# Optimization experiments

Measured on AMD Instinct MI355X. Metric: run time of the kernel, lower is better.

## Reference

```python
import jax, jax.numpy as jnp
import numpy as np

B = 1048576  # batch
A = 3        # number of actors in the ensemble


def _linear_params(key, out_d, in_d):
    """Stacked-over-actors torch.nn.Linear-style init: U(-1/sqrt(in), 1/sqrt(in))."""
    k1, k2 = jax.random.split(key)
    s = 1.0 / np.sqrt(in_d)
    W = jax.random.uniform(k1, (A, out_d, in_d), minval=-s, maxval=s, dtype=jnp.float32)
    b = jax.random.uniform(k2, (A, out_d), minval=-s, maxval=s, dtype=jnp.float32)
    return W, b


def setup_inputs() -> dict:
    key = jax.random.key(0)
    ks = jax.random.split(key, 10)
    spatial = jax.random.normal(ks[0], (B, 3, 9), dtype=jnp.float32)
    car_stats = jax.random.normal(ks[1], (B, 4), dtype=jnp.float32)  # unused by the model
    Wmx, bmx = _linear_params(ks[2], 10, 6)
    Wnx, bnx = _linear_params(ks[3], 10, 3)
    Wmy, bmy = _linear_params(ks[4], 10, 6)
    Wny, bny = _linear_params(ks[5], 10, 3)
    Wmz, bmz = _linear_params(ks[6], 5, 6)
    Wnz, bnz = _linear_params(ks[7], 5, 3)
    Wlin, blin = _linear_params(ks[8], 25, 25)
    Wout, bout = _linear_params(ks[9], 15, 25)
    return {
        "spatial": spatial, "car_stats": car_stats,
        "Wmx": Wmx, "bmx": bmx, "Wnx": Wnx, "bnx": bnx,
        "Wmy": Wmy, "bmy": bmy, "Wny": Wny, "bny": bny,
        "Wmz": Wmz, "bmz": bmz, "Wnz": Wnz, "bnz": bnz,
        "Wlin": Wlin, "blin": blin, "Wout": Wout, "bout": bout,
    }


def reference(spatial, car_stats,
              Wmx, bmx, Wnx, bnx,
              Wmy, bmy, Wny, bny,
              Wmz, bmz, Wnz, bnz,
              Wlin, blin, Wout, bout):
    # SimpleSpatialInput vectorized over the actor axis 'a':
    # (Linear(6->size)(s[:, :6])) * (Linear(3->size)(s[:, 6:9]))
    def proc(s, Wm, bm, Wn, bn):
        m = jnp.einsum('bi,aoi->bao', s[:, :6], Wm) + bm   # [B, A, size]
        n = jnp.einsum('bi,aoi->bao', s[:, 6:9], Wn) + bn  # [B, A, size]
        return m * n

    px = proc(spatial[:, 0], Wmx, bmx, Wnx, bnx)  # [B, A, 10]
    py = proc(spatial[:, 1], Wmy, bmy, Wny, bny)  # [B, A, 10]
    pz = proc(spatial[:, 2], Wmz, bmz, Wnz, bnz)  # [B, A, 5]
    ps = jnp.concatenate([px, py, pz], axis=-1)   # [B, A, 25]

    h = jnp.einsum('bad,aod->bao', ps, Wlin) + blin  # [B, A, 25]
    h = h / (1.0 + jnp.abs(h))                       # Softsign
    out = jnp.einsum('bad,aod->bao', h, Wout) + bout # [B, A, 15]

    result = jnp.transpose(out, (0, 2, 1))           # [B, 15, A] (stack dim=2)
    multiplier = jax.nn.softmax(result[:, 9, :], axis=1)  # [B, A]
    # stack of result[:, i] * multiplier over i=0..8, cumsum over actors,
    # take last -> plain weighted sum over the actor axis.
    return jnp.einsum('boa,ba->bo', result[:, :9, :], multiplier)  # [B, 9]
```

## Files before the change

### kernel.cpp

```cpp
#include <hip/hip_runtime.h>


typedef _Float16 half8  __attribute__((ext_vector_type(8)));
typedef float    floatx4 __attribute__((ext_vector_type(4)));

#define NFRAG 21
#define FRAG_HALFS (NFRAG * 512)
#define BIAS_FLOATS (NFRAG * 16)

__global__ __launch_bounds__(256) void prep_frags(
    const float* __restrict__ Wmx, const float* __restrict__ bmx,
    const float* __restrict__ Wnx, const float* __restrict__ bnx,
    const float* __restrict__ Wmy, const float* __restrict__ bmy,
    const float* __restrict__ Wny, const float* __restrict__ bny,
    const float* __restrict__ Wmz, const float* __restrict__ bmz,
    const float* __restrict__ Wnz, const float* __restrict__ bnz,
    const float* __restrict__ Wlin, const float* __restrict__ blin,
    const float* __restrict__ Wout, const float* __restrict__ bout,
    _Float16* __restrict__ frag, float* __restrict__ bias)
{
    int i = threadIdx.x + blockIdx.x * blockDim.x;
    if (i < FRAG_HALFS) {
        int f = i >> 9, rem = i & 511;
        int lane = rem >> 3, j = rem & 7;
        int q = lane >> 4, m = lane & 15;
        int a = f / 7, idx = f % 7;
        float v = 0.f;
        if (idx < 4) {
            int c = m + ((idx & 1) ? 16 : 0);
            int k = 8 * q + j;
            bool npart = (idx >= 2);
            if (c < 10) {
                if (!npart) { if (k < 6)             v = Wmx[(a*10 + c)*6 + k]; }
                else        { if (k >= 6 && k < 9)   v = Wnx[(a*10 + c)*3 + (k-6)]; }
            } else if (c < 20) {
                if (!npart) { if (k >= 9 && k < 15)  v = Wmy[(a*10 + c-10)*6 + (k-9)]; }
                else        { if (k >= 15 && k < 18) v = Wny[(a*10 + c-10)*3 + (k-15)]; }
            } else if (c < 25) {
                if (!npart) { if (k >= 18 && k < 24) v = Wmz[(a*5 + c-20)*6 + (k-18)]; }
                else        { if (k >= 24 && k < 27) v = Wnz[(a*5 + c-20)*3 + (k-24)]; }
            }
        } else if (idx < 6) {
            int o  = m + ((idx == 5) ? 16 : 0);
            int kc = 16 * (j >> 2) + 4 * q + (j & 3);
            if (o < 25 && kc < 25) v = Wlin[(a*25 + o)*25 + kc];
        } else {
            int ko = 16 * (j >> 2) + 4 * q + (j & 3);
            if (m < 10 && ko < 25) v = Wout[(a*15 + m)*25 + ko];
        }
        frag[(size_t)f * 512 + lane * 8 + j] = (_Float16)v;
    } else if (i < FRAG_HALFS + BIAS_FLOATS) {
        int r = i - FRAG_HALFS;
        int f = r >> 4, m = r & 15;
        int a = f / 7, idx = f % 7;
        float b = 0.f;
        if (idx < 4) {
            int c = m + ((idx & 1) ? 16 : 0);
            bool npart = (idx >= 2);
            if (c < 10)      b = npart ? bnx[a*10 + c]      : bmx[a*10 + c];
            else if (c < 20) b = npart ? bny[a*10 + c-10]   : bmy[a*10 + c-10];
            else if (c < 25) b = npart ? bnz[a*5 + c-20]    : bmz[a*5 + c-20];
        } else if (idx < 6) {
            int o = m + ((idx == 5) ? 16 : 0);
            if (o < 25) b = blin[a*25 + o];
        } else {
            if (m < 10) b = bout[a*15 + m];
        }
        bias[r] = b;
    }
}

__global__ __launch_bounds__(256) void actor_mfma(
    const float* __restrict__ spatial,
    const _Float16* __restrict__ frag,
    const float* __restrict__ bias,
    float* __restrict__ out)
{
    __shared__ float    lds_s[1728];
    __shared__ _Float16 lds_f[FRAG_HALFS];
    __shared__ float    lds_b[BIAS_FLOATS];

    const int t = threadIdx.x;
    const int lane = t & 63, w = t >> 6;
    const int q = lane >> 4, e = lane & 15;
    const size_t b0 = (size_t)blockIdx.x * 64;

    {
        const float4* g  = (const float4*)(spatial + b0 * 27);
        float4* d4 = (float4*)lds_s;
        d4[t] = g[t];
        if (t + 256 < 432) d4[t + 256] = g[t + 256];
        const float4* gf = (const float4*)frag;
        float4* df = (float4*)lds_f;
        #pragma unroll
        for (int k = 0; k < 6; ++k) {
            int idx = t + k * 256;
            if (idx < 1344) df[idx] = gf[idx];
        }
        const float4* gb = (const float4*)bias;
        float4* db = (float4*)lds_b;
        if (t < 84) db[t] = gb[t];
    }
    __syncthreads();

    half8 Bs;
    {
        const float* src = lds_s + (w * 16 + e) * 27 + 8 * q;
        #pragma unroll
        for (int j = 0; j < 8; ++j) {
            int k = 8 * q + j;
            Bs[j] = (_Float16)(k < 27 ? src[j] : 0.f);
        }
    }

    const half8*   fL = (const half8*)lds_f;
    const floatx4* bL = (const floatx4*)lds_b;

    floatx4 oacc[3];

    #pragma unroll
    for (int a = 0; a < 3; ++a) {
        const int fb = a * 7;
        floatx4 M0 = __builtin_amdgcn_mfma_f32_16x16x32_f16(fL[(fb+0)*64+lane], Bs, bL[(fb+0)*4+q], 0,0,0);
        floatx4 M1 = __builtin_amdgcn_mfma_f32_16x16x32_f16(fL[(fb+1)*64+lane], Bs, bL[(fb+1)*4+q], 0,0,0);
        floatx4 N0 = __builtin_amdgcn_mfma_f32_16x16x32_f16(fL[(fb+2)*64+lane], Bs, bL[(fb+2)*4+q], 0,0,0);
        floatx4 N1 = __builtin_amdgcn_mfma_f32_16x16x32_f16(fL[(fb+3)*64+lane], Bs, bL[(fb+3)*4+q], 0,0,0);

        half8 P;
        #pragma unroll
        for (int r = 0; r < 4; ++r) {
            P[r]     = (_Float16)(M0[r] * N0[r]);
            P[4 + r] = (_Float16)(M1[r] * N1[r]);
        }

        floatx4 H0 = __builtin_amdgcn_mfma_f32_16x16x32_f16(fL[(fb+4)*64+lane], P, bL[(fb+4)*4+q], 0,0,0);
        floatx4 H1 = __builtin_amdgcn_mfma_f32_16x16x32_f16(fL[(fb+5)*64+lane], P, bL[(fb+5)*4+q], 0,0,0);

        half8 Hh;
        #pragma unroll
        for (int r = 0; r < 4; ++r) {
            float v0 = H0[r];
            Hh[r]     = (_Float16)(v0 * __builtin_amdgcn_rcpf(1.0f + fabsf(v0)));
            float v1 = H1[r];
            Hh[4 + r] = (_Float16)(v1 * __builtin_amdgcn_rcpf(1.0f + fabsf(v1)));
        }

        oacc[a] = __builtin_amdgcn_mfma_f32_16x16x32_f16(fL[(fb+6)*64+lane], Hh, bL[(fb+6)*4+q], 0,0,0);
    }

    const int src9 = 32 + e;
    float g0 = __shfl(oacc[0][1], src9, 64);
    float g1 = __shfl(oacc[1][1], src9, 64);
    float g2 = __shfl(oacc[2][1], src9, 64);
    float mx = fmaxf(g0, fmaxf(g1, g2));
    float e0 = __expf(g0 - mx);
    float e1 = __expf(g1 - mx);
    float e2 = __expf(g2 - mx);
    float inv = __builtin_amdgcn_rcpf(e0 + e1 + e2);
    e0 *= inv; e1 *= inv; e2 *= inv;

    float res[4];
    #pragma unroll
    for (int r = 0; r < 4; ++r)
        res[r] = oacc[0][r] * e0 + oacc[1][r] * e1 + oacc[2][r] * e2;

    float* ldso = lds_s + w * 432;
    if (q < 2) {
        #pragma unroll
        for (int r = 0; r < 4; ++r) ldso[e * 9 + 4 * q + r] = res[r];
    } else if (q == 2) {
        ldso[e * 9 + 8] = res[0];
    }
    if (lane < 36) {
        float4 v = *(const float4*)(ldso + lane * 4);
        *(float4*)(out + (b0 + w * 16) * 9 + lane * 4) = v;
    }
}

extern "C" void kernel_launch(void* const* d_in, const int* in_sizes, int n_in,
                              void* d_out, int out_size, void* d_ws, size_t ws_size,
                              hipStream_t stream) {
    const float* spatial = (const float*)d_in[0];
    const float* Wmx  = (const float*)d_in[2];
    const float* bmx  = (const float*)d_in[3];
    const float* Wnx  = (const float*)d_in[4];
    const float* bnx  = (const float*)d_in[5];
    const float* Wmy  = (const float*)d_in[6];
    const float* bmy  = (const float*)d_in[7];
    const float* Wny  = (const float*)d_in[8];
    const float* bny  = (const float*)d_in[9];
    const float* Wmz  = (const float*)d_in[10];
    const float* bmz  = (const float*)d_in[11];
    const float* Wnz  = (const float*)d_in[12];
    const float* bnz  = (const float*)d_in[13];
    const float* Wlin = (const float*)d_in[14];
    const float* blin = (const float*)d_in[15];
    const float* Wout = (const float*)d_in[16];
    const float* bout = (const float*)d_in[17];
    float* out = (float*)d_out;

    _Float16* frag = (_Float16*)d_ws;
    float*    bias = (float*)((char*)d_ws + FRAG_HALFS * 2);

    prep_frags<<<dim3(44), dim3(256), 0, stream>>>(
        Wmx, bmx, Wnx, bnx, Wmy, bmy, Wny, bny, Wmz, bmz, Wnz, bnz,
        Wlin, blin, Wout, bout, frag, bias);

    const int nb = in_sizes[0] / 27;
    dim3 grid(nb / 64);
    actor_mfma<<<grid, dim3(256), 0, stream>>>(spatial, frag, bias, out);
}
```

Baseline: 258.0 us.

## Make MFMA kernel persistent over tiles with register-resident weights and folded biases

Each block now processes 16 tiles of 64 rows instead of one. The weight fragments are held in registers, loaded once per wave from global memory rather than staged through LDS by every block. Spatial rows are read straight from global with a two-tile software prefetch, so the next load overlaps the current tile's MFMAs. Biases are folded into the fragments as an extra K column fed by a constant 1 in the B operand, so the accumulator starts at zero and the separate bias buffer and loads are removed. The cost is heavy register pressure from 21 half8 fragments, fewer blocks in the grid, and strided uncoalesced per-lane global loads of spatial.

Result: no change. 258.6 us (+0.2%).

```diff
diff --git a/kernel.cpp b/kernel.cpp
--- a/kernel.cpp
+++ b/kernel.cpp
@@ -6,7 +6,7 @@
 
 #define NFRAG 21
 #define FRAG_HALFS (NFRAG * 512)
-#define BIAS_FLOATS (NFRAG * 16)
+#define TPB 16
 
 __global__ __launch_bounds__(256) void prep_frags(
     const float* __restrict__ Wmx, const float* __restrict__ bmx,
@@ -17,163 +17,157 @@
     const float* __restrict__ Wnz, const float* __restrict__ bnz,
     const float* __restrict__ Wlin, const float* __restrict__ blin,
     const float* __restrict__ Wout, const float* __restrict__ bout,
-    _Float16* __restrict__ frag, float* __restrict__ bias)
+    _Float16* __restrict__ frag)
 {
     int i = threadIdx.x + blockIdx.x * blockDim.x;
-    if (i < FRAG_HALFS) {
-        int f = i >> 9, rem = i & 511;
-        int lane = rem >> 3, j = rem & 7;
-        int q = lane >> 4, m = lane & 15;
-        int a = f / 7, idx = f % 7;
-        float v = 0.f;
-        if (idx < 4) {
-            int c = m + ((idx & 1) ? 16 : 0);
-            int k = 8 * q + j;
-            bool npart = (idx >= 2);
-            if (c < 10) {
-                if (!npart) { if (k < 6)             v = Wmx[(a*10 + c)*6 + k]; }
-                else        { if (k >= 6 && k < 9)   v = Wnx[(a*10 + c)*3 + (k-6)]; }
-            } else if (c < 20) {
-                if (!npart) { if (k >= 9 && k < 15)  v = Wmy[(a*10 + c-10)*6 + (k-9)]; }
-                else        { if (k >= 15 && k < 18) v = Wny[(a*10 + c-10)*3 + (k-15)]; }
-            } else if (c < 25) {
-                if (!npart) { if (k >= 18 && k < 24) v = Wmz[(a*5 + c-20)*6 + (k-18)]; }
-                else        { if (k >= 24 && k < 27) v = Wnz[(a*5 + c-20)*3 + (k-24)]; }
-            }
-        } else if (idx < 6) {
-            int o  = m + ((idx == 5) ? 16 : 0);
-            int kc = 16 * (j >> 2) + 4 * q + (j & 3);
-            if (o < 25 && kc < 25) v = Wlin[(a*25 + o)*25 + kc];
-        } else {
-            int ko = 16 * (j >> 2) + 4 * q + (j & 3);
-            if (m < 10 && ko < 25) v = Wout[(a*15 + m)*25 + ko];
-        }
-        frag[(size_t)f * 512 + lane * 8 + j] = (_Float16)v;
-    } else if (i < FRAG_HALFS + BIAS_FLOATS) {
-        int r = i - FRAG_HALFS;
-        int f = r >> 4, m = r & 15;
-        int a = f / 7, idx = f % 7;
-        float b = 0.f;
-        if (idx < 4) {
-            int c = m + ((idx & 1) ? 16 : 0);
-            bool npart = (idx >= 2);
-            if (c < 10)      b = npart ? bnx[a*10 + c]      : bmx[a*10 + c];
-            else if (c < 20) b = npart ? bny[a*10 + c-10]   : bmy[a*10 + c-10];
-            else if (c < 25) b = npart ? bnz[a*5 + c-20]    : bmz[a*5 + c-20];
-        } else if (idx < 6) {
-            int o = m + ((idx == 5) ? 16 : 0);
-            if (o < 25) b = blin[a*25 + o];
-        } else {
-            if (m < 10) b = bout[a*15 + m];
-        }
-        bias[r] = b;
+    if (i >= FRAG_HALFS) return;
+    int f = i >> 9, rem = i & 511;
+    int lane = rem >> 3, j = rem & 7;
+    int q = lane >> 4, m = lane & 15;
+    int a = f / 7, idx = f % 7;
+    float v = 0.f;
+    if (idx < 4) {
+        int c = m + ((idx & 1) ? 16 : 0);
+        int k = 8 * q + j;
+        bool npart = (idx >= 2);
+        if (c < 10) {
+            if (!npart) { if (k < 6)             v = Wmx[(a*10 + c)*6 + k];
+                          else if (k == 27)      v = bmx[a*10 + c]; }
+            else        { if (k >= 6 && k < 9)   v = Wnx[(a*10 + c)*3 + (k-6)];
+                          else if (k == 27)      v = bnx[a*10 + c]; }
+        } else if (c < 20) {
+            if (!npart) { if (k >= 9 && k < 15)  v = Wmy[(a*10 + c-10)*6 + (k-9)];
+                          else if (k == 27)      v = bmy[a*10 + c-10]; }
+            else        { if (k >= 15 && k < 18) v = Wny[(a*10 + c-10)*3 + (k-15)];
+                          else if (k == 27)      v = bny[a*10 + c-10]; }
+        } else if (c < 25) {
+            if (!npart) { if (k >= 18 && k < 24) v = Wmz[(a*5 + c-20)*6 + (k-18)];
+                          else if (k == 27)      v = bmz[a*5 + c-20]; }
+            else        { if (k >= 24 && k < 27) v = Wnz[(a*5 + c-20)*3 + (k-24)];
+                          else if (k == 27)      v = bnz[a*5 + c-20]; }
+        }
+    } else if (idx < 6) {
+        int o  = m + ((idx == 5) ? 16 : 0);
+        int kc = 16 * (j >> 2) + 4 * q + (j & 3);
+        if (o < 25) {
+            if (kc < 25)       v = Wlin[(a*25 + o)*25 + kc];
+            else if (kc == 25) v = blin[a*25 + o];
+        }
+    } else {
+        int ko = 16 * (j >> 2) + 4 * q + (j & 3);
+        if (m < 10) {
+            if (ko < 25)       v = Wout[(a*15 + m)*25 + ko];
+            else if (ko == 25) v = bout[a*15 + m];
+        }
     }
+    frag[(size_t)f * 512 + lane * 8 + j] = (_Float16)v;
 }
 
 __global__ __launch_bounds__(256) void actor_mfma(
     const float* __restrict__ spatial,
     const _Float16* __restrict__ frag,
-    const float* __restrict__ bias,
     float* __restrict__ out)
 {
-    __shared__ float    lds_s[1728];
-    __shared__ _Float16 lds_f[FRAG_HALFS];
-    __shared__ float    lds_b[BIAS_FLOATS];
+    __shared__ float lds_o[4 * 144];
 
     const int t = threadIdx.x;
     const int lane = t & 63, w = t >> 6;
     const int q = lane >> 4, e = lane & 15;
-    const size_t b0 = (size_t)blockIdx.x * 64;
-
-    {
-        const float4* g  = (const float4*)(spatial + b0 * 27);
-        float4* d4 = (float4*)lds_s;
-        d4[t] = g[t];
-        if (t + 256 < 432) d4[t + 256] = g[t + 256];
-        const float4* gf = (const float4*)frag;
-        float4* df = (float4*)lds_f;
-        #pragma unroll
-        for (int k = 0; k < 6; ++k) {
-            int idx = t + k * 256;
-            if (idx < 1344) df[idx] = gf[idx];
-        }
-        const float4* gb = (const float4*)bias;
-        float4* db = (float4*)lds_b;
-        if (t < 84) db[t] = gb[t];
-    }
-    __syncthreads();
-
-    half8 Bs;
-    {
-        const float* src = lds_s + (w * 16 + e) * 27 + 8 * q;
+    const size_t b0 = (size_t)blockIdx.x * (64 * TPB);
+
+    half8 F[NFRAG];
+    #pragma unroll
+    for (int f = 0; f < NFRAG; ++f)
+        F[f] = *(const half8*)(frag + (size_t)f * 512 + lane * 8);
+
+    const float* sbase = spatial + (b0 + (size_t)(w * 16 + e)) * 27 + 8 * q;
+    float* const ldso = lds_o + w * 144;
+    const floatx4 z = {0.f, 0.f, 0.f, 0.f};
+
+    auto loadT = [&](float (&dst)[8], int tt) {
+        const float* s_ = sbase + (size_t)tt * (64 * 27);
         #pragma unroll
         for (int j = 0; j < 8; ++j) {
             int k = 8 * q + j;
-            Bs[j] = (_Float16)(k < 27 ? src[j] : 0.f);
-        }
-    }
-
-    const half8*   fL = (const half8*)lds_f;
-    const floatx4* bL = (const floatx4*)lds_b;
-
-    floatx4 oacc[3];
-
-    #pragma unroll
-    for (int a = 0; a < 3; ++a) {
-        const int fb = a * 7;
-        floatx4 M0 = __builtin_amdgcn_mfma_f32_16x16x32_f16(fL[(fb+0)*64+lane], Bs, bL[(fb+0)*4+q], 0,0,0);
-        floatx4 M1 = __builtin_amdgcn_mfma_f32_16x16x32_f16(fL[(fb+1)*64+lane], Bs, bL[(fb+1)*4+q], 0,0,0);
-        floatx4 N0 = __builtin_amdgcn_mfma_f32_16x16x32_f16(fL[(fb+2)*64+lane], Bs, bL[(fb+2)*4+q], 0,0,0);
-        floatx4 N1 = __builtin_amdgcn_mfma_f32_16x16x32_f16(fL[(fb+3)*64+lane], Bs, bL[(fb+3)*4+q], 0,0,0);
-
-        half8 P;
-        #pragma unroll
-        for (int r = 0; r < 4; ++r) {
-            P[r]     = (_Float16)(M0[r] * N0[r]);
-            P[4 + r] = (_Float16)(M1[r] * N1[r]);
-        }
-
-        floatx4 H0 = __builtin_amdgcn_mfma_f32_16x16x32_f16(fL[(fb+4)*64+lane], P, bL[(fb+4)*4+q], 0,0,0);
-        floatx4 H1 = __builtin_amdgcn_mfma_f32_16x16x32_f16(fL[(fb+5)*64+lane], P, bL[(fb+5)*4+q], 0,0,0);
-
-        half8 Hh;
-        #pragma unroll
-        for (int r = 0; r < 4; ++r) {
-            float v0 = H0[r];
-            Hh[r]     = (_Float16)(v0 * __builtin_amdgcn_rcpf(1.0f + fabsf(v0)));
-            float v1 = H1[r];
-            Hh[4 + r] = (_Float16)(v1 * __builtin_amdgcn_rcpf(1.0f + fabsf(v1)));
-        }
-
-        oacc[a] = __builtin_amdgcn_mfma_f32_16x16x32_f16(fL[(fb+6)*64+lane], Hh, bL[(fb+6)*4+q], 0,0,0);
-    }
-
-    const int src9 = 32 + e;
-    float g0 = __shfl(oacc[0][1], src9, 64);
-    float g1 = __shfl(oacc[1][1], src9, 64);
-    float g2 = __shfl(oacc[2][1], src9, 64);
-    float mx = fmaxf(g0, fmaxf(g1, g2));
-    float e0 = __expf(g0 - mx);
-    float e1 = __expf(g1 - mx);
-    float e2 = __expf(g2 - mx);
-    float inv = __builtin_amdgcn_rcpf(e0 + e1 + e2);
-    e0 *= inv; e1 *= inv; e2 *= inv;
-
-    float res[4];
-    #pragma unroll
-    for (int r = 0; r < 4; ++r)
-        res[r] = oacc[0][r] * e0 + oacc[1][r] * e1 + oacc[2][r] * e2;
-
-    float* ldso = lds_s + w * 432;
-    if (q < 2) {
-        #pragma unroll
-        for (int r = 0; r < 4; ++r) ldso[e * 9 + 4 * q + r] = res[r];
-    } else if (q == 2) {
-        ldso[e * 9 + 8] = res[0];
-    }
-    if (lane < 36) {
-        float4 v = *(const float4*)(ldso + lane * 4);
-        *(float4*)(out + (b0 + w * 16) * 9 + lane * 4) = v;
+            float v = (k == 27) ? 1.f : 0.f;
+            if (k < 27) v = s_[j];
+            dst[j] = v;
+        }
+    };
+
+    auto tileCompute = [&](const float (&cur)[8], int tt) {
+        half8 Bs;
+        #pragma unroll
+        for (int j = 0; j < 8; ++j) Bs[j] = (_Float16)cur[j];
+
+        floatx4 oacc[3];
+        #pragma unroll
+        for (int a = 0; a < 3; ++a) {
+            const int fb = a * 7;
+            floatx4 M0 = __builtin_amdgcn_mfma_f32_16x16x32_f16(F[fb+0], Bs, z, 0,0,0);
+            floatx4 M1 = __builtin_amdgcn_mfma_f32_16x16x32_f16(F[fb+1], Bs, z, 0,0,0);
+            floatx4 N0 = __builtin_amdgcn_mfma_f32_16x16x32_f16(F[fb+2], Bs, z, 0,0,0);
+            floatx4 N1 = __builtin_amdgcn_mfma_f32_16x16x32_f16(F[fb+3], Bs, z, 0,0,0);
+
+            half8 P;
+            #pragma unroll
+            for (int r = 0; r < 4; ++r) {
+                P[r]     = (_Float16)(M0[r] * N0[r]);
+                P[4 + r] = (_Float16)(M1[r] * N1[r]);
+            }
+            if (q == 2) P[5] = (_Float16)1.f;
+
+            floatx4 H0 = __builtin_amdgcn_mfma_f32_16x16x32_f16(F[fb+4], P, z, 0,0,0);
+            floatx4 H1 = __builtin_amdgcn_mfma_f32_16x16x32_f16(F[fb+5], P, z, 0,0,0);
+
+            half8 Hh;
+            #pragma unroll
+            for (int r = 0; r < 4; ++r) {
+                float v0 = H0[r];
+                Hh[r]     = (_Float16)(v0 * __builtin_amdgcn_rcpf(1.0f + fabsf(v0)));
+                float v1 = H1[r];
+                Hh[4 + r] = (_Float16)(v1 * __builtin_amdgcn_rcpf(1.0f + fabsf(v1)));
+            }
+            if (q == 2) Hh[5] = (_Float16)1.f;
+
+            oacc[a] = __builtin_amdgcn_mfma_f32_16x16x32_f16(F[fb+6], Hh, z, 0,0,0);
+        }
+
+        const int src9 = 32 + e;
+        float g0 = __shfl(oacc[0][1], src9, 64);
+        float g1 = __shfl(oacc[1][1], src9, 64);
+        float g2 = __shfl(oacc[2][1], src9, 64);
+        float mx = fmaxf(g0, fmaxf(g1, g2));
+        float e0 = __expf(g0 - mx);
+        float e1 = __expf(g1 - mx);
+        float e2 = __expf(g2 - mx);
+        float inv = __builtin_amdgcn_rcpf(e0 + e1 + e2);
+        e0 *= inv; e1 *= inv; e2 *= inv;
+
+        float res[4];
+        #pragma unroll
+        for (int r = 0; r < 4; ++r)
+            res[r] = oacc[0][r] * e0 + oacc[1][r] * e1 + oacc[2][r] * e2;
+
+        if (q < 2) {
+            #pragma unroll
+            for (int r = 0; r < 4; ++r) ldso[e * 9 + 4 * q + r] = res[r];
+        } else if (q == 2) {
+            ldso[e * 9 + 8] = res[0];
+        }
+        if (lane < 36) {
+            float4 v = *(const float4*)(ldso + lane * 4);
+            *(float4*)(out + (b0 + (size_t)tt * 64 + w * 16) * 9 + lane * 4) = v;
+        }
+    };
+
+    float sA[8], sB[8];
+    loadT(sA, 0);
+    for (int tt = 0; tt < TPB; tt += 2) {
+        loadT(sB, tt + 1);
+        tileCompute(sA, tt);
+        if (tt + 2 < TPB) loadT(sA, tt + 2);
+        tileCompute(sB, tt + 1);
     }
 }
 
@@ -200,13 +194,12 @@
     float* out = (float*)d_out;
 
     _Float16* frag = (_Float16*)d_ws;
-    float*    bias = (float*)((char*)d_ws + FRAG_HALFS * 2);
-
-    prep_frags<<<dim3(44), dim3(256), 0, stream>>>(
+
+    prep_frags<<<dim3(42), dim3(256), 0, stream>>>(
         Wmx, bmx, Wnx, bnx, Wmy, bmy, Wny, bny, Wmz, bmz, Wnz, bnz,
-        Wlin, blin, Wout, bout, frag, bias);
+        Wlin, blin, Wout, bout, frag);
 
     const int nb = in_sizes[0] / 27;
-    dim3 grid(nb / 64);
-    actor_mfma<<<grid, dim3(256), 0, stream>>>(spatial, frag, bias, out);
+    dim3 grid(nb / (64 * TPB));
+    actor_mfma<<<grid, dim3(256), 0, stream>>>(spatial, frag, out);
 }
```
